# Optimization experiments

Measured on AMD Instinct MI355X. Metric: run time of the kernel, lower is better.

## Reference

```python
import jax, jax.numpy as jnp
import numpy as np

BN_EPS = 1e-5

def setup_inputs() -> dict:
    key = jax.random.key(0)
    k1, k2, k3 = jax.random.split(key, 3)
    N, E, D_IN, D_OUT = 65536, 1048576, 64, 64
    x = jax.random.normal(k1, (N, D_IN), dtype=jnp.float32)
    edge_index = jax.random.randint(k2, (2, E), 0, N, dtype=jnp.int64)
    W = jax.random.normal(k3, (D_IN, D_OUT), dtype=jnp.float32) / np.sqrt(D_IN)
    b = jnp.zeros((D_OUT,), dtype=jnp.float32)
    gamma = jnp.ones((D_OUT,), dtype=jnp.float32)
    beta = jnp.zeros((D_OUT,), dtype=jnp.float32)
    return {"x": x, "edge_index": edge_index, "W": W, "b": b, "gamma": gamma, "beta": beta}

def reference(x, edge_index, W, b, gamma, beta):
    N = x.shape[0]
    loop = jnp.arange(N, dtype=edge_index.dtype)
    src = jnp.concatenate([edge_index[0], loop])  # source nodes j (with self-loops)
    dst = jnp.concatenate([edge_index[1], loop])  # target nodes i
    # symmetric GCN normalization: deg from in-edges incl. self-loops
    deg = jax.ops.segment_sum(jnp.ones(dst.shape, dtype=x.dtype), dst, num_segments=N)
    dinv = jax.lax.rsqrt(deg)  # deg >= 1 thanks to self-loops
    h = x @ W                              # [N, D_OUT]
    norm = dinv[src] * dinv[dst]           # [E+N]
    msg = h[src] * norm[:, None]           # gather + scale
    agg = jax.ops.segment_sum(msg, dst, num_segments=N) + b  # scatter-add
    # BatchNorm1d (training mode: batch statistics over nodes)
    mean = jnp.mean(agg, axis=0)
    var = jnp.mean(jnp.square(agg - mean), axis=0)
    y = gamma * (agg - mean) * jax.lax.rsqrt(var + BN_EPS) + beta
    return jax.nn.relu(y)
```

## Files before the change

kernel.cpp:

```cpp
#include <hip/hip_runtime.h>

#define THREADS 256
#define SEG 4096
#define AT_LD 68
#define BN_EPS 1e-5f
#define NREP 8
#define GATHER_BLOCKS 2048

__device__ __forceinline__ float bf2f(ushort u) {
    return __uint_as_float(((unsigned)u) << 16);
}
__device__ __forceinline__ ushort f2bf(float f) {
    unsigned b = __float_as_uint(f);
    return (ushort)((b + 0x7FFFu + ((b >> 16) & 1u)) >> 16);
}

__global__ __launch_bounds__(THREADS) void init_kernel(int* __restrict__ bcursor, int cap,
                                                       float* __restrict__ stats_rep) {
    int t = threadIdx.x;
    bcursor[t] = t * cap;
#pragma unroll
    for (int r = 0; r < 4; ++r) stats_rep[r * THREADS + t] = 0.f;
}

__global__ __launch_bounds__(THREADS) void conv_part_kernel(const int* __restrict__ src,
                                                            const int* __restrict__ dst, int E,
                                                            int nPart,
                                                            int* __restrict__ bcursor,
                                                            unsigned* __restrict__ staging,
                                                            const float* __restrict__ x,
                                                            const float* __restrict__ W,
                                                            ushort* __restrict__ xh, int N) {
    __shared__ __align__(16) char smem[64 * AT_LD * 4 + 64 * 64 * 4];
    int bid = blockIdx.x;
    int tid = threadIdx.x;
    if (bid < nPart) {
        int* hist = (int*)smem;
        int* gbase = hist + 256;
        int* lcnt = gbase + 256;
        int nseg = (E + SEG - 1) / SEG;
        for (int seg = bid; seg < nseg; seg += nPart) {
            int base = seg * SEG;
            int lim = min(E, base + SEG);
            hist[tid] = 0;
            __syncthreads();
            for (int i = base + tid; i < lim; i += THREADS)
                atomicAdd(&hist[dst[i] >> 8], 1);
            __syncthreads();
            if (hist[tid] > 0) gbase[tid] = atomicAdd(&bcursor[tid], hist[tid]);
            lcnt[tid] = 0;
            __syncthreads();
            for (int i = base + tid; i < lim; i += THREADS) {
                int d = dst[i];
                int b = d >> 8;
                int p = gbase[b] + atomicAdd(&lcnt[b], 1);
                staging[p] = (unsigned)src[i] | ((unsigned)(d & 255) << 16);
            }
            __syncthreads();
        }
    } else {
        float* Wl = (float*)smem;
        float* At = Wl + 4096;
        int tile = bid - nPart;
        for (int i = tid; i < 1024; i += THREADS)
            ((float4*)Wl)[i] = ((const float4*)W)[i];

        int c0 = (tid & 15) * 4;
        int r0 = (tid >> 4) * 4;
        int base = tile << 6;

        __syncthreads();
        for (int g = tid; g < 1024; g += THREADS) {
            int r = g >> 4, cc = (g & 15) << 2;
            int rowi = base + r;
            float4 v = {0.f, 0.f, 0.f, 0.f};
            if (rowi < N) v = *(const float4*)(x + ((size_t)rowi << 6) + cc);
            *(float4*)(&At[r * AT_LD + cc]) = v;
        }
        __syncthreads();

        float acc[4][4] = {};
#pragma unroll 1
        for (int k0 = 0; k0 < 64; k0 += 4) {
            float4 a[4], wf[4];
#pragma unroll
            for (int i = 0; i < 4; ++i)
                a[i] = *(const float4*)(&At[(r0 + i) * AT_LD + k0]);
#pragma unroll
            for (int q = 0; q < 4; ++q)
                wf[q] = *(const float4*)(&Wl[(k0 + q) * 64 + c0]);
#pragma unroll
            for (int i = 0; i < 4; ++i) {
                const float* ap = (const float*)&a[i];
#pragma unroll
                for (int j = 0; j < 4; ++j) {
                    acc[i][j] += ap[0] * ((const float*)&wf[0])[j] +
                                 ap[1] * ((const float*)&wf[1])[j] +
                                 ap[2] * ((const float*)&wf[2])[j] +
                                 ap[3] * ((const float*)&wf[3])[j];
                }
            }
        }

#pragma unroll
        for (int i = 0; i < 4; ++i) {
            int rowi = base + r0 + i;
            if (rowi < N) {
                ushort4 o = make_ushort4(f2bf(acc[i][0]), f2bf(acc[i][1]), f2bf(acc[i][2]),
                                         f2bf(acc[i][3]));
                *(ushort4*)(xh + ((size_t)rowi << 6) + c0) = o;
            }
        }
    }
}

__global__ __launch_bounds__(THREADS) void bucket_build_kernel(const unsigned* __restrict__ staging,
                                                               const int* __restrict__ bcursor,
                                                               int cap, int N,
                                                               int* __restrict__ deg,
                                                               int* __restrict__ offs,
                                                               float* __restrict__ dinv,
                                                               int* __restrict__ csr) {
    __shared__ int hist[256];
    __shared__ int lofs[256];
    __shared__ int lcur[256];
    int tid = threadIdx.x;
    int b = blockIdx.x;
    int s = b * cap;
    int e = bcursor[b];

    hist[tid] = 0;
    __syncthreads();
    for (int i = s + tid; i < e; i += THREADS)
        atomicAdd(&hist[staging[i] >> 16], 1);
    __syncthreads();

    int v = hist[tid];
    lofs[tid] = v;
    __syncthreads();
    for (int off = 1; off < 256; off <<= 1) {
        int u = (tid >= off) ? lofs[tid - off] : 0;
        __syncthreads();
        lofs[tid] += u;
        __syncthreads();
    }
    int excl = lofs[tid] - v;

    int node = (b << 8) + tid;
    if (node < N) {
        deg[node] = v;
        offs[node] = s + excl;
        dinv[node] = rsqrtf((float)v + 1.0f);
    }
    lcur[tid] = excl;
    __syncthreads();

    for (int i = s + tid; i < e; i += THREADS) {
        unsigned w = staging[i];
        int ln = (int)(w >> 16);
        int p = atomicAdd(&lcur[ln], 1);
        csr[s + p] = (int)(w & 0xFFFFu);
    }
}

__global__ __launch_bounds__(THREADS) void gather_stats_kernel(const ushort* __restrict__ xh,
                                                               const int* __restrict__ offs,
                                                               const int* __restrict__ deg,
                                                               const int* __restrict__ csr,
                                                               const float* __restrict__ dinv,
                                                               float* __restrict__ out,
                                                               float* __restrict__ stats_rep,
                                                               int N) {
    __shared__ float bred[128];
    int tid = threadIdx.x;
    int lane = tid & 63;
    if (tid < 128) bred[tid] = 0.f;
    __syncthreads();

    int wid = (blockIdx.x * THREADS + tid) >> 6;
    int nwaves = (gridDim.x * THREADS) >> 6;
    float fsum = 0.f, fsq = 0.f;

    for (int nd = wid; nd < N; nd += nwaves) {
        int node = __builtin_amdgcn_readfirstlane(nd);
        float dd = dinv[node];
        float acc = dd * bf2f(xh[((size_t)node << 6) + lane]);
        int start = offs[node];
        int cnt = deg[node];
        const int* __restrict__ row = csr + start;
        int j = 0;
        for (; j + 16 <= cnt; j += 16) {
            int s[16];
            float w[16];
            ushort u[16];
#pragma unroll
            for (int q = 0; q < 16; ++q) s[q] = __builtin_amdgcn_readfirstlane(row[j + q]);
#pragma unroll
            for (int q = 0; q < 16; ++q) w[q] = dinv[s[q]];
#pragma unroll
            for (int q = 0; q < 16; ++q) u[q] = xh[((size_t)s[q] << 6) + lane];
#pragma unroll
            for (int q = 0; q < 16; ++q) acc += w[q] * bf2f(u[q]);
        }
        for (; j + 4 <= cnt; j += 4) {
            int s[4];
            float w[4];
            ushort u[4];
#pragma unroll
            for (int q = 0; q < 4; ++q) s[q] = __builtin_amdgcn_readfirstlane(row[j + q]);
#pragma unroll
            for (int q = 0; q < 4; ++q) w[q] = dinv[s[q]];
#pragma unroll
            for (int q = 0; q < 4; ++q) u[q] = xh[((size_t)s[q] << 6) + lane];
#pragma unroll
            for (int q = 0; q < 4; ++q) acc += w[q] * bf2f(u[q]);
        }
        for (; j < cnt; ++j) {
            int s = __builtin_amdgcn_readfirstlane(row[j]);
            acc += dinv[s] * bf2f(xh[((size_t)s << 6) + lane]);
        }
        float h = dd * acc;
        out[((size_t)node << 6) + lane] = h;
        fsum += h;
        fsq += h * h;
    }

    atomicAdd(&bred[lane], fsum);
    atomicAdd(&bred[64 + lane], fsq);
    __syncthreads();
    if (tid < 128)
        atomicAdd(&stats_rep[((blockIdx.x & (NREP - 1)) << 7) + tid], bred[tid]);
}

__global__ __launch_bounds__(THREADS) void bn_relu_kernel(float* __restrict__ io,
                                                          const float* __restrict__ stats_rep,
                                                          const float* __restrict__ gamma,
                                                          const float* __restrict__ beta,
                                                          int n4, float invN) {
    __shared__ float sc[64];
    __shared__ float sh[64];
    int tid = threadIdx.x;
    if (tid < 64) {
        float s1 = 0.f, s2 = 0.f;
#pragma unroll
        for (int r = 0; r < NREP; ++r) {
            s1 += stats_rep[(r << 7) + tid];
            s2 += stats_rep[(r << 7) + 64 + tid];
        }
        float mean = s1 * invN;
        float var = s2 * invN - mean * mean;
        float scale = gamma[tid] * rsqrtf(var + BN_EPS);
        sc[tid] = scale;
        sh[tid] = beta[tid] - mean * scale;
    }
    __syncthreads();

    int t = blockIdx.x * blockDim.x + tid;
    if (t >= n4) return;
    int f0 = (t & 15) * 4;
    float4 v = ((const float4*)io)[t];
    float vv[4] = {v.x, v.y, v.z, v.w};
    float o[4];
#pragma unroll
    for (int j = 0; j < 4; ++j) {
        float y = vv[j] * sc[f0 + j] + sh[f0 + j];
        o[j] = y > 0.f ? y : 0.f;
    }
    float4 r = {o[0], o[1], o[2], o[3]};
    ((float4*)io)[t] = r;
}

__global__ __launch_bounds__(THREADS) void deg_kernel(const int* __restrict__ dst, int E,
                                                      int* __restrict__ deg) {
    int e = blockIdx.x * blockDim.x + threadIdx.x;
    if (e < E) atomicAdd(&deg[dst[e]], 1);
}

__global__ __launch_bounds__(THREADS) void dinv_kernel(const int* __restrict__ deg,
                                                       float* __restrict__ dinv, int N) {
    int i = blockIdx.x * blockDim.x + threadIdx.x;
    if (i < N) dinv[i] = rsqrtf((float)deg[i] + 1.0f);
}

__global__ __launch_bounds__(THREADS) void selfloop_kernel(const float4* __restrict__ x4,
                                                           const float* __restrict__ dinv,
                                                           float4* __restrict__ out4, int n4) {
    int t = blockIdx.x * blockDim.x + threadIdx.x;
    if (t >= n4) return;
    int node = t >> 4;
    float s = dinv[node];
    s *= s;
    float4 v = x4[t];
    v.x *= s; v.y *= s; v.z *= s; v.w *= s;
    out4[t] = v;
}

__global__ __launch_bounds__(THREADS) void scatter_kernel(const int* __restrict__ src,
                                                          const int* __restrict__ dst, int E,
                                                          const float* __restrict__ x,
                                                          const float* __restrict__ dinv,
                                                          float* __restrict__ out) {
    int lane = threadIdx.x & 63;
    int wave = (blockIdx.x * blockDim.x + threadIdx.x) >> 6;
    int nwaves = (gridDim.x * blockDim.x) >> 6;
    for (int e = wave; e < E; e += nwaves) {
        int s = src[e];
        int d = dst[e];
        float nrm = dinv[s] * dinv[d];
        atomicAdd(&out[d * 64 + lane], x[s * 64 + lane] * nrm);
    }
}

__global__ __launch_bounds__(THREADS) void matmul_stats_kernel(float* __restrict__ io,
                                                               const float* __restrict__ W,
                                                               float* __restrict__ stats, int N) {
    __shared__ float Wl[64 * 64];
    __shared__ float At[64 * AT_LD];
    __shared__ float bred[128];
    int tid = threadIdx.x;

    for (int i = tid; i < 1024; i += THREADS)
        ((float4*)Wl)[i] = ((const float4*)W)[i];

    int c0 = (tid & 15) * 4;
    int r0 = (tid >> 4) * 4;
    int ntiles = (N + 63) >> 6;
    float sums[4] = {0.f, 0.f, 0.f, 0.f};
    float sqs[4] = {0.f, 0.f, 0.f, 0.f};

    for (int tile = blockIdx.x; tile < ntiles; tile += gridDim.x) {
        int base = tile << 6;
        __syncthreads();
        for (int g = tid; g < 1024; g += THREADS) {
            int r = g >> 4, cc = (g & 15) << 2;
            int rowi = base + r;
            float4 v = {0.f, 0.f, 0.f, 0.f};
            if (rowi < N) v = *(const float4*)(io + ((size_t)rowi << 6) + cc);
            *(float4*)(&At[r * AT_LD + cc]) = v;
        }
        __syncthreads();

        float acc[4][4] = {};
#pragma unroll 1
        for (int k0 = 0; k0 < 64; k0 += 4) {
            float4 a[4], wf[4];
#pragma unroll
            for (int i = 0; i < 4; ++i)
                a[i] = *(const float4*)(&At[(r0 + i) * AT_LD + k0]);
#pragma unroll
            for (int q = 0; q < 4; ++q)
                wf[q] = *(const float4*)(&Wl[(k0 + q) * 64 + c0]);
#pragma unroll
            for (int i = 0; i < 4; ++i) {
                const float* ap = (const float*)&a[i];
#pragma unroll
                for (int j = 0; j < 4; ++j) {
                    acc[i][j] += ap[0] * ((const float*)&wf[0])[j] +
                                 ap[1] * ((const float*)&wf[1])[j] +
                                 ap[2] * ((const float*)&wf[2])[j] +
                                 ap[3] * ((const float*)&wf[3])[j];
                }
            }
        }

#pragma unroll
        for (int i = 0; i < 4; ++i) {
            int rowi = base + r0 + i;
            if (rowi < N) {
                float4 o = {acc[i][0], acc[i][1], acc[i][2], acc[i][3]};
                *(float4*)(io + ((size_t)rowi << 6) + c0) = o;
#pragma unroll
                for (int j = 0; j < 4; ++j) {
                    sums[j] += acc[i][j];
                    sqs[j] += acc[i][j] * acc[i][j];
                }
            }
        }
    }

    __syncthreads();
    if (tid < 128) bred[tid] = 0.f;
    __syncthreads();
#pragma unroll
    for (int j = 0; j < 4; ++j) {
        atomicAdd(&bred[c0 + j], sums[j]);
        atomicAdd(&bred[64 + c0 + j], sqs[j]);
    }
    __syncthreads();
    if (tid < 128) atomicAdd(&stats[tid], bred[tid]);
}

extern "C" void kernel_launch(void* const* d_in, const int* in_sizes, int n_in,
                              void* d_out, int out_size, void* d_ws, size_t ws_size,
                              hipStream_t stream) {
    const float* x     = (const float*)d_in[0];
    const int*   edges = (const int*)d_in[1];
    const float* W     = (const float*)d_in[2];
    const float* gamma = (const float*)d_in[4];
    const float* beta  = (const float*)d_in[5];
    float* out = (float*)d_out;

    const int N = in_sizes[0] / 64;
    const int E = in_sizes[1] / 2;
    const int* src = edges;
    const int* dst = edges + E;
    const int n4 = N * 16;

    const int nb = (N + 255) >> 8;
    const int avg = (E + nb - 1) / nb;
    const int cap = avg + (avg >> 2) + 512;

    char* ws = (char*)d_ws;
    size_t off_stats   = 0;
    size_t off_bcursor = 4096;
    size_t off_deg     = off_bcursor + 1024;
    size_t off_offs    = off_deg + (size_t)4 * N;
    size_t off_dinv    = off_offs + (size_t)4 * N;
    size_t off_csr     = off_dinv + (size_t)4 * N;
    size_t off_staging = off_csr + (size_t)4 * nb * cap;
    size_t off_xh      = (off_staging + (size_t)4 * nb * cap + 15) & ~(size_t)15;
    size_t need        = off_xh + (size_t)128 * N;

    if (ws_size >= need && N <= 65536) {
        float* stats_rep = (float*)(ws + off_stats);
        int*   bcursor   = (int*)(ws + off_bcursor);
        int*   deg       = (int*)(ws + off_deg);
        int*   offs      = (int*)(ws + off_offs);
        float* dinv      = (float*)(ws + off_dinv);
        int*   csr       = (int*)(ws + off_csr);
        unsigned* staging = (unsigned*)(ws + off_staging);
        ushort* xh       = (ushort*)(ws + off_xh);

        int nseg = (E + SEG - 1) / SEG;
        int nPart = nseg < 1024 ? nseg : 1024;
        int ntiles = (N + 63) >> 6;

        init_kernel<<<1, THREADS, 0, stream>>>(bcursor, cap, stats_rep);
        conv_part_kernel<<<nPart + ntiles, THREADS, 0, stream>>>(
            src, dst, E, nPart, bcursor, staging, x, W, xh, N);
        bucket_build_kernel<<<nb, THREADS, 0, stream>>>(staging, bcursor, cap, N, deg, offs,
                                                        dinv, csr);
        gather_stats_kernel<<<GATHER_BLOCKS, THREADS, 0, stream>>>(xh, offs, deg, csr, dinv,
                                                                   out, stats_rep, N);
        bn_relu_kernel<<<(n4 + THREADS - 1) / THREADS, THREADS, 0, stream>>>(
            out, stats_rep, gamma, beta, n4, 1.0f / (float)N);
    } else {
        int*   deg   = (int*)ws;
        float* stats = (float*)(ws + (size_t)N * 4);
        float* dinv  = (float*)(ws + (size_t)N * 4 + 4096);

        hipMemsetAsync(ws, 0, (size_t)N * 4 + 4096, stream);
        deg_kernel<<<(E + THREADS - 1) / THREADS, THREADS, 0, stream>>>(dst, E, deg);
        dinv_kernel<<<(N + THREADS - 1) / THREADS, THREADS, 0, stream>>>(deg, dinv, N);
        selfloop_kernel<<<(n4 + THREADS - 1) / THREADS, THREADS, 0, stream>>>(
            (const float4*)x, dinv, (float4*)out, n4);
        scatter_kernel<<<1024, THREADS, 0, stream>>>(src, dst, E, x, dinv, out);
        matmul_stats_kernel<<<512, THREADS, 0, stream>>>(out, W, stats, N);
        bn_relu_kernel<<<(n4 + THREADS - 1) / THREADS, THREADS, 0, stream>>>(
            out, stats, gamma, beta, n4, 1.0f / (float)N);
    }
}
```

Baseline: 118.0 us.

## Launch one wave per node in gather kernel and widen stats replicas

Replaces the persistent grid-stride gather loop (2048 blocks) with a grid that assigns exactly one wavefront per node, so hardware block scheduling handles load balance. Raises the number of replicated BN-statistics buffers from 8 to 32 to spread the higher count of per-block global atomics, and makes bn_relu reduce the replicas with 128 threads through shared memory. In exchange, every block now does a shared-memory reduction plus 128 global atomics for only four nodes. The reduction also writes past the 64-entry `sc` array on the assumption that `sh` sits right after it in shared memory.

After: 116.0 us. Within noise of the previous version (-1.7%).

```diff
diff --git a/kernel.cpp b/kernel.cpp
--- a/kernel.cpp
+++ b/kernel.cpp
@@ -4,8 +4,7 @@
 #define SEG 4096
 #define AT_LD 68
 #define BN_EPS 1e-5f
-#define NREP 8
-#define GATHER_BLOCKS 2048
+#define NREP 32
 
 __device__ __forceinline__ float bf2f(ushort u) {
     return __uint_as_float(((unsigned)u) << 16);
@@ -20,7 +19,7 @@
     int t = threadIdx.x;
     bcursor[t] = t * cap;
 #pragma unroll
-    for (int r = 0; r < 4; ++r) stats_rep[r * THREADS + t] = 0.f;
+    for (int r = 0; r < NREP / 2; ++r) stats_rep[r * THREADS + t] = 0.f;
 }
 
 __global__ __launch_bounds__(THREADS) void conv_part_kernel(const int* __restrict__ src,
@@ -177,12 +176,9 @@
     if (tid < 128) bred[tid] = 0.f;
     __syncthreads();
 
-    int wid = (blockIdx.x * THREADS + tid) >> 6;
-    int nwaves = (gridDim.x * THREADS) >> 6;
-    float fsum = 0.f, fsq = 0.f;
-
-    for (int nd = wid; nd < N; nd += nwaves) {
-        int node = __builtin_amdgcn_readfirstlane(nd);
+    int node = __builtin_amdgcn_readfirstlane((int)((blockIdx.x * THREADS + tid) >> 6));
+    float h = 0.f;
+    if (node < N) {
         float dd = dinv[node];
         float acc = dd * bf2f(xh[((size_t)node << 6) + lane]);
         int start = offs[node];
@@ -219,14 +215,12 @@
             int s = __builtin_amdgcn_readfirstlane(row[j]);
             acc += dinv[s] * bf2f(xh[((size_t)s << 6) + lane]);
         }
-        float h = dd * acc;
+        h = dd * acc;
         out[((size_t)node << 6) + lane] = h;
-        fsum += h;
-        fsq += h * h;
-    }
-
-    atomicAdd(&bred[lane], fsum);
-    atomicAdd(&bred[64 + lane], fsq);
+    }
+
+    atomicAdd(&bred[lane], h);
+    atomicAdd(&bred[64 + lane], h * h);
     __syncthreads();
     if (tid < 128)
         atomicAdd(&stats_rep[((blockIdx.x & (NREP - 1)) << 7) + tid], bred[tid]);
@@ -240,13 +234,17 @@
     __shared__ float sc[64];
     __shared__ float sh[64];
     int tid = threadIdx.x;
+    if (tid < 128) {
+        float s = 0.f;
+#pragma unroll
+        for (int r = 0; r < NREP; ++r) s += stats_rep[(r << 7) + tid];
+        bred_store:;
+        ((float*)sc)[tid] = s;
+    }
+    __syncthreads();
     if (tid < 64) {
-        float s1 = 0.f, s2 = 0.f;
-#pragma unroll
-        for (int r = 0; r < NREP; ++r) {
-            s1 += stats_rep[(r << 7) + tid];
-            s2 += stats_rep[(r << 7) + 64 + tid];
-        }
+        float s1 = sc[tid];
+        float s2 = sh[tid];
         float mean = s1 * invN;
         float var = s2 * invN - mean * mean;
         float scale = gamma[tid] * rsqrtf(var + BN_EPS);
@@ -412,7 +410,7 @@
 
     char* ws = (char*)d_ws;
     size_t off_stats   = 0;
-    size_t off_bcursor = 4096;
+    size_t off_bcursor = (size_t)NREP * 128 * 4;
     size_t off_deg     = off_bcursor + 1024;
     size_t off_offs    = off_deg + (size_t)4 * N;
     size_t off_dinv    = off_offs + (size_t)4 * N;
@@ -440,16 +438,16 @@
             src, dst, E, nPart, bcursor, staging, x, W, xh, N);
         bucket_build_kernel<<<nb, THREADS, 0, stream>>>(staging, bcursor, cap, N, deg, offs,
                                                         dinv, csr);
-        gather_stats_kernel<<<GATHER_BLOCKS, THREADS, 0, stream>>>(xh, offs, deg, csr, dinv,
-                                                                   out, stats_rep, N);
+        gather_stats_kernel<<<(N * 64 + THREADS - 1) / THREADS, THREADS, 0, stream>>>(
+            xh, offs, deg, csr, dinv, out, stats_rep, N);
         bn_relu_kernel<<<(n4 + THREADS - 1) / THREADS, THREADS, 0, stream>>>(
             out, stats_rep, gamma, beta, n4, 1.0f / (float)N);
     } else {
         int*   deg   = (int*)ws;
         float* stats = (float*)(ws + (size_t)N * 4);
-        float* dinv  = (float*)(ws + (size_t)N * 4 + 4096);
-
-        hipMemsetAsync(ws, 0, (size_t)N * 4 + 4096, stream);
+        float* dinv  = (float*)(ws + (size_t)N * 4 + (size_t)NREP * 128 * 4);
+
+        hipMemsetAsync(ws, 0, (size_t)N * 4 + (size_t)NREP * 128 * 4, stream);
         deg_kernel<<<(E + THREADS - 1) / THREADS, THREADS, 0, stream>>>(dst, E, deg);
         dinv_kernel<<<(N + THREADS - 1) / THREADS, THREADS, 0, stream>>>(deg, dinv, N);
         selfloop_kernel<<<(n4 + THREADS - 1) / THREADS, THREADS, 0, stream>>>(
```
